# Kernel tuning notes

Hardware: AMD Instinct MI355X
Metric: run time of the kernel (lower is better)

Reference implementation:

```python
import jax, jax.numpy as jnp
import numpy as np

B, S, D = 64, 512, 768  # batch, max wordpieces (BERT max pos), hidden dim


def setup_inputs() -> dict:
    key = jax.random.key(0)
    k_emb, k_seg = jax.random.split(key)
    # last_hidden_state from the (frozen) BERT backbone
    embeddings = jax.random.normal(k_emb, (B, S, D), dtype=jnp.float32)
    # word-group id per wordpiece token, non-decreasing within each row
    # (token i belongs to word segment_ids[b, i]; '##' continuations share
    #  the id of their head wordpiece, mirroring aggregate_tokens)
    segment_ids = jnp.sort(
        jax.random.randint(k_seg, (B, S), 0, S, dtype=jnp.int32), axis=-1
    )
    return {"embeddings": embeddings, "segment_ids": segment_ids}


def reference(embeddings, segment_ids):
    # Vectorized equivalent of BertEncoder.aggregate_tokens + head slicing:
    # sum wordpiece embeddings within each word group, zero-pad to S words.
    n, s, d = embeddings.shape
    agg = jax.vmap(
        lambda e, seg: jax.ops.segment_sum(e, seg, num_segments=s)
    )(embeddings, segment_ids)  # [B, S, D], trailing unused slots are zeros
    report_feat = agg[:, 0]      # [B, D]   ([CLS] word embedding)
    word_feat = agg[:, 1:]       # [B, S-1, D]
    return report_feat, word_feat
```

## Files before the change

### kernel.cpp

```cpp
#include <hip/hip_runtime.h>


constexpr int B  = 64;
constexpr int S  = 512;
constexpr int D  = 768;
constexpr int D4 = D / 4;
constexpr int G  = 4;
constexpr int WPB = S / G;
constexpr int BLOCK = 256;

__global__ __launch_bounds__(BLOCK) void segsum_g4_kernel(
    const float4* __restrict__ emb,
    const int*    __restrict__ seg,
    float4*       __restrict__ out) {
  const int wave = (blockIdx.x * BLOCK + threadIdx.x) >> 6;
  const int lane = threadIdx.x & 63;
  const int b    = wave >> 7;
  const int g0   = (wave & (WPB - 1)) * G;

  const int4* row = (const int4*)(seg + b * S);
  const int4 a0 = row[lane];
  const int4 a1 = row[lane + 64];

  int pref[G + 1];
#pragma unroll
  for (int j = 0; j <= G; ++j) {
    const int t = g0 + j;
    int c = 0;
    c += __popcll(__ballot(a0.x < t));
    c += __popcll(__ballot(a0.y < t));
    c += __popcll(__ballot(a0.z < t));
    c += __popcll(__ballot(a0.w < t));
    c += __popcll(__ballot(a1.x < t));
    c += __popcll(__ballot(a1.y < t));
    c += __popcll(__ballot(a1.z < t));
    c += __popcll(__ballot(a1.w < t));
    pref[j] = c;
  }

  const float4* p = emb + ((size_t)b * S + pref[0]) * D4 + lane;
#pragma unroll
  for (int j = 0; j < G; ++j) {
    float4 acc0 = make_float4(0.f, 0.f, 0.f, 0.f);
    float4 acc1 = acc0, acc2 = acc0;
    for (int k = pref[j]; k < pref[j + 1]; ++k) {
      float4 e0 = p[0], e1 = p[64], e2 = p[128];
      acc0.x += e0.x; acc0.y += e0.y; acc0.z += e0.z; acc0.w += e0.w;
      acc1.x += e1.x; acc1.y += e1.y; acc1.z += e1.z; acc1.w += e1.w;
      acc2.x += e2.x; acc2.y += e2.y; acc2.z += e2.z; acc2.w += e2.w;
      p += D4;
    }
    const int g = g0 + j;
    float4* dst = (g == 0)
        ? out + (size_t)b * D4
        : out + (size_t)B * D4 + ((size_t)b * (S - 1) + (g - 1)) * D4;
    dst[lane]       = acc0;
    dst[lane + 64]  = acc1;
    dst[lane + 128] = acc2;
  }
}

extern "C" void kernel_launch(void* const* d_in, const int* in_sizes, int n_in,
                              void* d_out, int out_size, void* d_ws, size_t ws_size,
                              hipStream_t stream) {
  const float4* emb = (const float4*)d_in[0];
  const int*    seg = (const int*)d_in[1];
  float4*       out = (float4*)d_out;

  const int waves  = B * S / G;
  const int blocks = waves / (BLOCK / 64);
  segsum_g4_kernel<<<blocks, BLOCK, 0, stream>>>(emb, seg, out);
}
```

Before: 184.5 us.

## Restructure segment sum as block-wide row scan with batched loads

Each block of 192 threads now owns 16 consecutive segments of one batch row. Every thread owns one float4 column. The block streams through the covered embedding rows in batches of 8 independent loads, flushing the accumulator at each segment boundary found in a shared-memory prefix table. Before, each wave handled 4 segments with a serial dependent load loop per segment. The new layout is meant to expose more memory-level parallelism and to keep the loop length independent of segment sizes. In exchange it adds a __syncthreads, clamped redundant loads at batch tails, and data-dependent branching in the flush loop.

```diff
diff --git a/kernel.cpp b/kernel.cpp
--- a/kernel.cpp
+++ b/kernel.cpp
@@ -5,27 +5,37 @@
 constexpr int S  = 512;
 constexpr int D  = 768;
 constexpr int D4 = D / 4;
-constexpr int G  = 4;
-constexpr int WPB = S / G;
-constexpr int BLOCK = 256;
+constexpr int VALS    = 16;
+constexpr int THREADS = 192;
+constexpr int WPB     = S / VALS;
+constexpr int NBLK    = B * WPB;
 
-__global__ __launch_bounds__(BLOCK) void segsum_g4_kernel(
+__device__ __forceinline__ void facc(float4& a, const float4& e) {
+  a.x += e.x; a.y += e.y; a.z += e.z; a.w += e.w;
+}
+
+__device__ __forceinline__ float4* out_row(float4* out, int b, int g) {
+  return (g == 0) ? out + (size_t)b * D4
+                  : out + (size_t)B * D4 + ((size_t)b * (S - 1) + (g - 1)) * D4;
+}
+
+__global__ __launch_bounds__(THREADS, 6) void segsum_scan_kernel(
     const float4* __restrict__ emb,
     const int*    __restrict__ seg,
     float4*       __restrict__ out) {
-  const int wave = (blockIdx.x * BLOCK + threadIdx.x) >> 6;
-  const int lane = threadIdx.x & 63;
-  const int b    = wave >> 7;
-  const int g0   = (wave & (WPB - 1)) * G;
+  const int b    = blockIdx.x >> 5;
+  const int v0   = (blockIdx.x & (WPB - 1)) * VALS;
+  const int tid  = threadIdx.x;
+  const int lane = tid & 63;
+  const int wav  = tid >> 6;
+
+  __shared__ int s_pref[VALS + 1];
 
   const int4* row = (const int4*)(seg + b * S);
   const int4 a0 = row[lane];
   const int4 a1 = row[lane + 64];
-
-  int pref[G + 1];
-#pragma unroll
-  for (int j = 0; j <= G; ++j) {
-    const int t = g0 + j;
+  for (int j = wav; j <= VALS; j += 3) {
+    const int t = v0 + j;
     int c = 0;
     c += __popcll(__ballot(a0.x < t));
     c += __popcll(__ballot(a0.y < t));
@@ -35,28 +45,43 @@
     c += __popcll(__ballot(a1.y < t));
     c += __popcll(__ballot(a1.z < t));
     c += __popcll(__ballot(a1.w < t));
-    pref[j] = c;
+    if (lane == 0) s_pref[j] = c;
+  }
+  __syncthreads();
+
+  const int rbeg = s_pref[0];
+  const int rend = s_pref[VALS];
+
+  const float4* base = emb + (size_t)b * S * D4 + tid;
+  float4 acc = make_float4(0.f, 0.f, 0.f, 0.f);
+  int v   = 0;
+  int nxt = s_pref[1];
+
+  for (int r = rbeg; r < rend; r += 8) {
+    float4 e[8];
+#pragma unroll
+    for (int u = 0; u < 8; ++u) {
+      int rr = r + u;
+      rr = rr < rend ? rr : rend - 1;
+      e[u] = base[(size_t)rr * D4];
+    }
+#pragma unroll
+    for (int u = 0; u < 8; ++u) {
+      const int rr = r + u;
+      if (rr >= rend) break;
+      while (rr == nxt) {
+        out_row(out, b, v0 + v)[tid] = acc;
+        acc = make_float4(0.f, 0.f, 0.f, 0.f);
+        ++v;
+        nxt = s_pref[v + 1];
+      }
+      facc(acc, e[u]);
+    }
   }
 
-  const float4* p = emb + ((size_t)b * S + pref[0]) * D4 + lane;
-#pragma unroll
-  for (int j = 0; j < G; ++j) {
-    float4 acc0 = make_float4(0.f, 0.f, 0.f, 0.f);
-    float4 acc1 = acc0, acc2 = acc0;
-    for (int k = pref[j]; k < pref[j + 1]; ++k) {
-      float4 e0 = p[0], e1 = p[64], e2 = p[128];
-      acc0.x += e0.x; acc0.y += e0.y; acc0.z += e0.z; acc0.w += e0.w;
-      acc1.x += e1.x; acc1.y += e1.y; acc1.z += e1.z; acc1.w += e1.w;
-      acc2.x += e2.x; acc2.y += e2.y; acc2.z += e2.z; acc2.w += e2.w;
-      p += D4;
-    }
-    const int g = g0 + j;
-    float4* dst = (g == 0)
-        ? out + (size_t)b * D4
-        : out + (size_t)B * D4 + ((size_t)b * (S - 1) + (g - 1)) * D4;
-    dst[lane]       = acc0;
-    dst[lane + 64]  = acc1;
-    dst[lane + 128] = acc2;
+  for (; v < VALS; ++v) {
+    out_row(out, b, v0 + v)[tid] = acc;
+    acc = make_float4(0.f, 0.f, 0.f, 0.f);
   }
 }
 
@@ -66,8 +91,5 @@
   const float4* emb = (const float4*)d_in[0];
   const int*    seg = (const int*)d_in[1];
   float4*       out = (float4*)d_out;
-
-  const int waves  = B * S / G;
-  const int blocks = waves / (BLOCK / 64);
-  segsum_g4_kernel<<<blocks, BLOCK, 0, stream>>>(emb, seg, out);
+  segsum_scan_kernel<<<NBLK, THREADS, 0, stream>>>(emb, seg, out);
 }
```

New measurement: 183.7 us. No clear change (-0.4%).
